# Performance work log

Hardware: AMD Instinct MI355X
Metric: run time of the kernel (lower is better)

## Reference

```python
import jax, jax.numpy as jnp
import numpy as np

B, N, C_IN = 4, 2048, 64
HID, HEADS, NQ = 128, 4, 16
D = HID // HEADS  # per-head dim = 32
NEG_SLOPE = 0.2
MASK_VAL = -1e9


def setup_inputs() -> dict:
    key = jax.random.key(0)
    ks = jax.random.split(key, 8)
    x = jax.random.normal(ks[0], (B, N, C_IN), dtype=jnp.float32)
    adj = jax.random.randint(ks[1], (N, N), 0, 2, dtype=jnp.int32)
    # lin_in: Linear(in_channels, hidden_dim)
    W_in = jax.random.normal(ks[2], (C_IN, HID), dtype=jnp.float32) / np.sqrt(C_IN)
    b_in = jnp.zeros((HID,), dtype=jnp.float32)
    # attention vectors [1, heads, d]
    att_src = jax.random.normal(ks[3], (1, HEADS, D), dtype=jnp.float32) * 0.1
    att_dst = jax.random.normal(ks[4], (1, HEADS, D), dtype=jnp.float32) * 0.1
    # output_head: Linear(num_nodes*hidden_dim, num_qubits)
    W_out = jax.random.normal(ks[5], (N * HID, NQ), dtype=jnp.float32) / np.sqrt(N * HID)
    b_out = jnp.zeros((NQ,), dtype=jnp.float32)
    return {"x": x, "adj": adj, "W_in": W_in, "b_in": b_in,
            "att_src": att_src, "att_dst": att_dst,
            "W_out": W_out, "b_out": b_out}


def reference(x, adj, W_in, b_in, att_src, att_dst, W_out, b_out):
    b, n, _ = x.shape
    h = (x @ W_in + b_in).reshape(b, n, HEADS, D)          # [B,N,H,D]
    alpha_src = jnp.sum(h * att_src, axis=-1)               # [B,N,H]
    alpha_dst = jnp.sum(h * att_dst, axis=-1)               # [B,N,H]
    # additive scores: score[b,i,j,h] = src[b,i,h] + dst[b,j,h]
    scores = alpha_src[:, :, None, :] + alpha_dst[:, None, :, :]  # [B,N,N,H]
    scores = jnp.where(scores >= 0, scores, NEG_SLOPE * scores)   # leaky relu
    mask = (adj == 0)[None, :, :, None]                     # [1,N,N,1]
    scores = jnp.where(mask, MASK_VAL, scores)
    alpha = jax.nn.softmax(scores, axis=2)                  # softmax over neighbors j
    # dropout p=0.0 (eval) -> identity
    out = jnp.einsum('bijh,bjhd->bihd', alpha, h)           # [B,N,H,D]
    out = out.reshape(b, n * HEADS * D)                     # [B, N*HID]
    return out @ W_out + b_out                              # [B, NQ]
```

## Files before the change

kernel.cpp:

```cpp
#include <hip/hip_runtime.h>
#include <math.h>

#define BB 4
#define NN 2048
#define CIN 64
#define HID 128
#define HEADS 4
#define DD 32
#define NQ 16
#define KTOT (NN*HID)
#define CCH 256
#define LOG2E 1.44269504088896340736f
#define NEGBIG -100.0f

typedef __attribute__((ext_vector_type(8))) _Float16 half8;
typedef __attribute__((ext_vector_type(2))) _Float16 half2;
typedef __attribute__((ext_vector_type(4))) float f32x4;

__global__ __launch_bounds__(256) void k_hidden(
    const float* __restrict__ x, const float* __restrict__ W_in,
    const float* __restrict__ b_in, const float* __restrict__ att_src,
    const float* __restrict__ att_dst, _Float16* __restrict__ hH,
    float* __restrict__ srcA, float* __restrict__ dstA)
{
    __shared__ float Wl[CIN * HID];
    __shared__ float xl[16][CIN];
    const int t = threadIdx.x;
    const int jj0 = blockIdx.x * 16;

    {
        const float4* Ws = (const float4*)W_in;
        float4* Wd = (float4*)Wl;
#pragma unroll
        for (int u = 0; u < 8; ++u) Wd[t + 256 * u] = Ws[t + 256 * u];
        ((float4*)&xl[0][0])[t] = ((const float4*)(x + (size_t)jj0 * CIN))[t];
    }
    __syncthreads();

    const int c = t & 127, rg = t >> 7;
    const int b = jj0 >> 11, j0 = jj0 & (NN - 1);
    const int h = c >> 5;

    float acc[8];
    const float bc = b_in[c];
#pragma unroll
    for (int rr = 0; rr < 8; ++rr) acc[rr] = bc;

#pragma unroll
    for (int k4 = 0; k4 < CIN; k4 += 4) {
        const float w0 = Wl[(k4 + 0) * HID + c];
        const float w1 = Wl[(k4 + 1) * HID + c];
        const float w2 = Wl[(k4 + 2) * HID + c];
        const float w3 = Wl[(k4 + 3) * HID + c];
#pragma unroll
        for (int rr = 0; rr < 8; ++rr) {
            const float4 xv = *(const float4*)&xl[rg * 8 + rr][k4];
            acc[rr] = fmaf(xv.w, w3, fmaf(xv.z, w2, fmaf(xv.y, w1, fmaf(xv.x, w0, acc[rr]))));
        }
    }

    half8 hv;
#pragma unroll
    for (int rr = 0; rr < 8; ++rr) hv[rr] = (_Float16)acc[rr];
    *(half8*)(hH + (size_t)(b * HID + c) * NN + j0 + rg * 8) = hv;

    const float as = att_src[c], ad = att_dst[c];
#pragma unroll
    for (int rr = 0; rr < 8; ++rr) {
        float vs = acc[rr] * as, vd = acc[rr] * ad;
#pragma unroll
        for (int m = 16; m >= 1; m >>= 1) {
            vs += __shfl_xor(vs, m, 64);
            vd += __shfl_xor(vd, m, 64);
        }
        if ((t & 31) == 0) {
            srcA[(size_t)(b * HEADS + h) * NN + j0 + rg * 8 + rr] = vs;
            dstA[(size_t)(b * HEADS + h) * NN + j0 + rg * 8 + rr] = vd;
        }
    }
}

__global__ __launch_bounds__(256) void k_adjb(const int* __restrict__ adj,
                                              unsigned* __restrict__ adjb)
{
    const int wid = blockIdx.x * 4 + (threadIdx.x >> 6);
    const int lane = threadIdx.x & 63;
    const int i = wid >> 5;
    const int jc = wid & 31;
    const int a = adj[(size_t)i * NN + jc * 64 + lane];
    const unsigned long long m = __ballot(a != 0);
    if (lane == 0) {
        *(uint2*)(adjb + (size_t)i * (NN / 32) + jc * 2) =
            make_uint2((unsigned)m, (unsigned)(m >> 32));
    }
}

__global__ __launch_bounds__(512, 4) void k_attn(
    const unsigned* __restrict__ adjb, const _Float16* __restrict__ hH,
    const float* __restrict__ srcA, const float* __restrict__ dstA,
    float* __restrict__ attO)
{
    __shared__ float ldst[HEADS][NN];
    __shared__ float redA[8][16][36];
    __shared__ float redS[8][16];

    const int t = threadIdx.x;
    const int lane = t & 63;
    const int w = t >> 6;
    const int h = w & 3;
    const int jh = w >> 2;
    const int b = blockIdx.x >> 7;
    const int i0 = (blockIdx.x & 127) * 16;

    {
        const float4* s4 = (const float4*)(dstA + (size_t)(b * HEADS + h) * NN + jh * 1024);
        float4* d4 = (float4*)&ldst[h][jh * 1024];
#pragma unroll
        for (int u = 0; u < 4; ++u) {
            float4 v = s4[lane + 64 * u];
            v.x *= LOG2E; v.y *= LOG2E; v.z *= LOG2E; v.w *= LOG2E;
            d4[lane + 64 * u] = v;
        }
    }

    const int r16 = lane & 15;
    const int g = lane >> 4;
    const float srci = srcA[(size_t)(b * HEADS + h) * NN + i0 + r16] * LOG2E;
    const uint2* adjrow2 = (const uint2*)(adjb + (size_t)(i0 + r16) * (NN / 32)) + jh * 16;
    const _Float16* bbase = hH + ((size_t)(b * HID) + h * DD + r16) * NN + jh * 1024 + 8 * g;

    f32x4 acc0 = {0.f, 0.f, 0.f, 0.f};
    f32x4 acc1 = {0.f, 0.f, 0.f, 0.f};
    f32x4 accS = {0.f, 0.f, 0.f, 0.f};
    const half8 ones = {(_Float16)1.f, (_Float16)1.f, (_Float16)1.f, (_Float16)1.f,
                        (_Float16)1.f, (_Float16)1.f, (_Float16)1.f, (_Float16)1.f};

    for (int jt2 = 0; jt2 < 1024; jt2 += 64) {
        const uint2 aw2 = adjrow2[jt2 >> 6];
#pragma unroll
        for (int s2 = 0; s2 < 2; ++s2) {
            const int jt = jt2 + 32 * s2;
            const unsigned bits = (s2 ? aw2.y : aw2.x) >> (8 * g);
            const float* dp = &ldst[h][jh * 1024 + jt + 8 * g];
            const float4 dl0 = *(const float4*)dp;
            const float4 dl1 = *(const float4*)(dp + 4);
            const half8 b0 = *(const half8*)(bbase + jt);
            const half8 b1 = *(const half8*)(bbase + 16 * NN + jt);
            const float dv[8] = {dl0.x, dl0.y, dl0.z, dl0.w, dl1.x, dl1.y, dl1.z, dl1.w};
            float wv[8];
#pragma unroll
            for (int e = 0; e < 8; ++e) {
                float s = srci + dv[e];
                s = fmaxf(s, 0.2f * s);
                s = (bits & (1u << e)) ? s : NEGBIG;
                wv[e] = __builtin_amdgcn_exp2f(s);
            }
            const half2 p0 = __builtin_bit_cast(half2, __builtin_amdgcn_cvt_pkrtz(wv[0], wv[1]));
            const half2 p1 = __builtin_bit_cast(half2, __builtin_amdgcn_cvt_pkrtz(wv[2], wv[3]));
            const half2 p2 = __builtin_bit_cast(half2, __builtin_amdgcn_cvt_pkrtz(wv[4], wv[5]));
            const half2 p3 = __builtin_bit_cast(half2, __builtin_amdgcn_cvt_pkrtz(wv[6], wv[7]));
            half8 af;
            af[0] = p0[0]; af[1] = p0[1]; af[2] = p1[0]; af[3] = p1[1];
            af[4] = p2[0]; af[5] = p2[1]; af[6] = p3[0]; af[7] = p3[1];
            acc0 = __builtin_amdgcn_mfma_f32_16x16x32_f16(af, b0, acc0, 0, 0, 0);
            acc1 = __builtin_amdgcn_mfma_f32_16x16x32_f16(af, b1, acc1, 0, 0, 0);
            accS = __builtin_amdgcn_mfma_f32_16x16x32_f16(af, ones, accS, 0, 0, 0);
        }
    }

#pragma unroll
    for (int r = 0; r < 4; ++r) {
        redA[w][4 * g + r][r16]      = acc0[r];
        redA[w][4 * g + r][16 + r16] = acc1[r];
    }
    if (r16 == 0) {
#pragma unroll
        for (int r = 0; r < 4; ++r) redS[w][4 * g + r] = accS[r];
    }
    __syncthreads();

    {
        const int i = t >> 5;
        const int q = t & 31;
        const int h2 = q >> 3;
        const int d0 = (q & 7) * 4;
        const float4 v0 = *(const float4*)&redA[h2][i][d0];
        const float4 v1 = *(const float4*)&redA[h2 + 4][i][d0];
        const float rs = redS[h2][i] + redS[h2 + 4][i];
        const float inv = __builtin_amdgcn_rcpf(rs);
        float4 o;
        o.x = (v0.x + v1.x) * inv; o.y = (v0.y + v1.y) * inv;
        o.z = (v0.z + v1.z) * inv; o.w = (v0.w + v1.w) * inv;
        *(float4*)(attO + (size_t)(b * NN + i0 + i) * HID + h2 * DD + d0) = o;
    }
}

__global__ void k_init(const float* __restrict__ b_out, float* __restrict__ dout)
{
    const int t = threadIdx.x;
    dout[t] = b_out[t & 15];
}

__global__ __launch_bounds__(256) void k_proj(
    const float* __restrict__ attO, const float* __restrict__ W_out,
    float* __restrict__ dout)
{
    const int t = threadIdx.x;
    const int k0 = blockIdx.x * (KTOT / CCH);

    float acc[64];
#pragma unroll
    for (int r = 0; r < 64; ++r) acc[r] = 0.f;

    for (int s = 0; s < (KTOT / CCH) / 256; ++s) {
        const int k = k0 + s * 256 + t;
        float a[4];
#pragma unroll
        for (int b = 0; b < 4; ++b) a[b] = attO[(size_t)b * KTOT + k];
        const float4* wr = (const float4*)(W_out + (size_t)k * NQ);
        float wf[16];
#pragma unroll
        for (int q4 = 0; q4 < 4; ++q4) {
            const float4 w4 = wr[q4];
            wf[q4 * 4 + 0] = w4.x; wf[q4 * 4 + 1] = w4.y;
            wf[q4 * 4 + 2] = w4.z; wf[q4 * 4 + 3] = w4.w;
        }
#pragma unroll
        for (int b = 0; b < 4; ++b)
#pragma unroll
            for (int q = 0; q < 16; ++q)
                acc[b * 16 + q] = fmaf(a[b], wf[q], acc[b * 16 + q]);
    }

    const int lane = t & 63, wave = t >> 6;
    __shared__ float red[4][64];
#pragma unroll
    for (int r = 0; r < 64; ++r) {
        float v = acc[r];
        v += __shfl_down(v, 32, 64);
        v += __shfl_down(v, 16, 64);
        v += __shfl_down(v, 8, 64);
        v += __shfl_down(v, 4, 64);
        v += __shfl_down(v, 2, 64);
        v += __shfl_down(v, 1, 64);
        if (lane == 0) red[wave][r] = v;
    }
    __syncthreads();
    if (t < 64) {
        const float v = red[0][t] + red[1][t] + red[2][t] + red[3][t];
        atomicAdd(&dout[t], v);
    }
}

extern "C" void kernel_launch(void* const* d_in, const int* in_sizes, int n_in,
                              void* d_out, int out_size, void* d_ws, size_t ws_size,
                              hipStream_t stream)
{
    const float* x       = (const float*)d_in[0];
    const int*   adj     = (const int*)d_in[1];
    const float* W_in    = (const float*)d_in[2];
    const float* b_in    = (const float*)d_in[3];
    const float* att_src = (const float*)d_in[4];
    const float* att_dst = (const float*)d_in[5];
    const float* W_out   = (const float*)d_in[6];
    const float* b_out   = (const float*)d_in[7];
    float* out = (float*)d_out;

    float* ws = (float*)d_ws;
    float* attO = ws;
    float* srcA = ws + (size_t)BB * HID * NN;
    float* dstA = srcA + (size_t)BB * HEADS * NN;
    _Float16* hH = (_Float16*)(dstA + (size_t)BB * HEADS * NN);
    unsigned* adjbw = (unsigned*)((char*)hH + sizeof(_Float16) * (size_t)BB * HID * NN);

    k_hidden<<<BB * NN / 16, 256, 0, stream>>>(x, W_in, b_in, att_src, att_dst, hH, srcA, dstA);
    k_adjb<<<NN * (NN / 64) / 4, 256, 0, stream>>>(adj, adjbw);
    k_attn<<<BB * (NN / 16), 512, 0, stream>>>(adjbw, hH, srcA, dstA, attO);
    k_init<<<1, 64, 0, stream>>>(b_out, out);
    k_proj<<<CCH, 256, 0, stream>>>(attO, W_out, out);
}
```

Measured before the change: 88.10 us.

## Split attention over neighbor halves, defer normalization to projection, fold init

The attention kernel's neighbor range is split across two blocks, doubling the grid, and its shared-memory dst staging is removed in favour of direct global loads with prefetched B and dst operands. Each half writes unnormalized fp16 partial outputs plus row sums. The projection kernel then combines both halves, normalizes and applies W_out, using one block per 512 K-elements. The LOG2E scaling moves into k_hidden, and output bias init is folded into k_adjb, removing a launch. The aim is more parallelism and occupancy in attention and fewer launches, at the cost of extra fp16 partial traffic, reduced precision, and many more atomics in the projection.

```diff
diff --git a/kernel.cpp b/kernel.cpp
--- a/kernel.cpp
+++ b/kernel.cpp
@@ -9,11 +9,11 @@
 #define DD 32
 #define NQ 16
 #define KTOT (NN*HID)
-#define CCH 256
 #define LOG2E 1.44269504088896340736f
 #define NEGBIG -100.0f
 
 typedef __attribute__((ext_vector_type(8))) _Float16 half8;
+typedef __attribute__((ext_vector_type(4))) _Float16 half4;
 typedef __attribute__((ext_vector_type(2))) _Float16 half2;
 typedef __attribute__((ext_vector_type(4))) float f32x4;
 
@@ -74,15 +74,18 @@
             vd += __shfl_xor(vd, m, 64);
         }
         if ((t & 31) == 0) {
-            srcA[(size_t)(b * HEADS + h) * NN + j0 + rg * 8 + rr] = vs;
-            dstA[(size_t)(b * HEADS + h) * NN + j0 + rg * 8 + rr] = vd;
+            srcA[(size_t)(b * HEADS + h) * NN + j0 + rg * 8 + rr] = vs * LOG2E;
+            dstA[(size_t)(b * HEADS + h) * NN + j0 + rg * 8 + rr] = vd * LOG2E;
         }
     }
 }
 
 __global__ __launch_bounds__(256) void k_adjb(const int* __restrict__ adj,
-                                              unsigned* __restrict__ adjb)
-{
+                                              unsigned* __restrict__ adjb,
+                                              const float* __restrict__ b_out,
+                                              float* __restrict__ dout)
+{
+    if (blockIdx.x == 0 && threadIdx.x < 64) dout[threadIdx.x] = b_out[threadIdx.x & 15];
     const int wid = blockIdx.x * 4 + (threadIdx.x >> 6);
     const int lane = threadIdx.x & 63;
     const int i = wid >> 5;
@@ -95,12 +98,11 @@
     }
 }
 
-__global__ __launch_bounds__(512, 4) void k_attn(
+__global__ __launch_bounds__(512, 8) void k_attn(
     const unsigned* __restrict__ adjb, const _Float16* __restrict__ hH,
     const float* __restrict__ srcA, const float* __restrict__ dstA,
-    float* __restrict__ attO)
-{
-    __shared__ float ldst[HEADS][NN];
+    _Float16* __restrict__ P, float* __restrict__ S)
+{
     __shared__ float redA[8][16][36];
     __shared__ float redS[8][16];
 
@@ -108,26 +110,18 @@
     const int lane = t & 63;
     const int w = t >> 6;
     const int h = w & 3;
-    const int jh = w >> 2;
-    const int b = blockIdx.x >> 7;
-    const int i0 = (blockIdx.x & 127) * 16;
-
-    {
-        const float4* s4 = (const float4*)(dstA + (size_t)(b * HEADS + h) * NN + jh * 1024);
-        float4* d4 = (float4*)&ldst[h][jh * 1024];
-#pragma unroll
-        for (int u = 0; u < 4; ++u) {
-            float4 v = s4[lane + 64 * u];
-            v.x *= LOG2E; v.y *= LOG2E; v.z *= LOG2E; v.w *= LOG2E;
-            d4[lane + 64 * u] = v;
-        }
-    }
+    const int bx = blockIdx.x;
+    const int jh = bx >> 9;
+    const int b = (bx >> 7) & 3;
+    const int i0 = (bx & 127) * 16;
+    const int jstart = jh * 1024 + (w >> 2) * 512;
 
     const int r16 = lane & 15;
     const int g = lane >> 4;
-    const float srci = srcA[(size_t)(b * HEADS + h) * NN + i0 + r16] * LOG2E;
-    const uint2* adjrow2 = (const uint2*)(adjb + (size_t)(i0 + r16) * (NN / 32)) + jh * 16;
-    const _Float16* bbase = hH + ((size_t)(b * HID) + h * DD + r16) * NN + jh * 1024 + 8 * g;
+    const float srci = srcA[(size_t)(b * HEADS + h) * NN + i0 + r16];
+    const uint2* adjrow2 = (const uint2*)(adjb + (size_t)(i0 + r16) * (NN / 32)) + (jstart >> 6);
+    const _Float16* bbase = hH + ((size_t)(b * HID) + h * DD + r16) * NN + jstart + 8 * g;
+    const float4* dst4 = (const float4*)(dstA + (size_t)(b * HEADS + h) * NN + jstart) + 2 * g;
 
     f32x4 acc0 = {0.f, 0.f, 0.f, 0.f};
     f32x4 acc1 = {0.f, 0.f, 0.f, 0.f};
@@ -135,18 +129,23 @@
     const half8 ones = {(_Float16)1.f, (_Float16)1.f, (_Float16)1.f, (_Float16)1.f,
                         (_Float16)1.f, (_Float16)1.f, (_Float16)1.f, (_Float16)1.f};
 
-    for (int jt2 = 0; jt2 < 1024; jt2 += 64) {
-        const uint2 aw2 = adjrow2[jt2 >> 6];
+    for (int it = 0; it < 8; ++it) {
+        const uint2 aw2 = adjrow2[it];
+        const half8 b0a = *(const half8*)(bbase + it * 64);
+        const half8 b0b = *(const half8*)(bbase + it * 64 + 32);
+        const half8 b1a = *(const half8*)(bbase + 16 * NN + it * 64);
+        const half8 b1b = *(const half8*)(bbase + 16 * NN + it * 64 + 32);
+        const float4 d0a = dst4[it * 16];
+        const float4 d0b = dst4[it * 16 + 1];
+        const float4 d1a = dst4[it * 16 + 8];
+        const float4 d1b = dst4[it * 16 + 9];
+
 #pragma unroll
         for (int s2 = 0; s2 < 2; ++s2) {
-            const int jt = jt2 + 32 * s2;
             const unsigned bits = (s2 ? aw2.y : aw2.x) >> (8 * g);
-            const float* dp = &ldst[h][jh * 1024 + jt + 8 * g];
-            const float4 dl0 = *(const float4*)dp;
-            const float4 dl1 = *(const float4*)(dp + 4);
-            const half8 b0 = *(const half8*)(bbase + jt);
-            const half8 b1 = *(const half8*)(bbase + 16 * NN + jt);
-            const float dv[8] = {dl0.x, dl0.y, dl0.z, dl0.w, dl1.x, dl1.y, dl1.z, dl1.w};
+            const float4 da = s2 ? d1a : d0a;
+            const float4 db = s2 ? d1b : d0b;
+            const float dv[8] = {da.x, da.y, da.z, da.w, db.x, db.y, db.z, db.w};
             float wv[8];
 #pragma unroll
             for (int e = 0; e < 8; ++e) {
@@ -162,8 +161,10 @@
             half8 af;
             af[0] = p0[0]; af[1] = p0[1]; af[2] = p1[0]; af[3] = p1[1];
             af[4] = p2[0]; af[5] = p2[1]; af[6] = p3[0]; af[7] = p3[1];
-            acc0 = __builtin_amdgcn_mfma_f32_16x16x32_f16(af, b0, acc0, 0, 0, 0);
-            acc1 = __builtin_amdgcn_mfma_f32_16x16x32_f16(af, b1, acc1, 0, 0, 0);
+            const half8 bb0 = s2 ? b0b : b0a;
+            const half8 bb1 = s2 ? b1b : b1a;
+            acc0 = __builtin_amdgcn_mfma_f32_16x16x32_f16(af, bb0, acc0, 0, 0, 0);
+            acc1 = __builtin_amdgcn_mfma_f32_16x16x32_f16(af, bb1, acc1, 0, 0, 0);
             accS = __builtin_amdgcn_mfma_f32_16x16x32_f16(af, ones, accS, 0, 0, 0);
         }
     }
@@ -186,50 +187,49 @@
         const int d0 = (q & 7) * 4;
         const float4 v0 = *(const float4*)&redA[h2][i][d0];
         const float4 v1 = *(const float4*)&redA[h2 + 4][i][d0];
-        const float rs = redS[h2][i] + redS[h2 + 4][i];
+        const half2 lo = __builtin_bit_cast(half2, __builtin_amdgcn_cvt_pkrtz(v0.x + v1.x, v0.y + v1.y));
+        const half2 hi = __builtin_bit_cast(half2, __builtin_amdgcn_cvt_pkrtz(v0.z + v1.z, v0.w + v1.w));
+        half4 o; o[0] = lo[0]; o[1] = lo[1]; o[2] = hi[0]; o[3] = hi[1];
+        *(half4*)(P + ((size_t)(jh * BB + b) * NN + i0 + i) * HID + h2 * DD + d0) = o;
+        if ((q & 7) == 0)
+            S[((size_t)(jh * BB + b) * NN + i0 + i) * HEADS + h2] = redS[h2][i] + redS[h2 + 4][i];
+    }
+}
+
+__global__ __launch_bounds__(256) void k_proj(
+    const _Float16* __restrict__ P, const float* __restrict__ S,
+    const float* __restrict__ W_out, float* __restrict__ dout)
+{
+    const int t = threadIdx.x;
+    const int k = blockIdx.x * 512 + t * 2;
+    const int i = k >> 7;
+    const int h = (k >> 5) & 3;
+
+    float wf0[16], wf1[16];
+    {
+        const float4* wr = (const float4*)(W_out + (size_t)k * NQ);
+#pragma unroll
+        for (int q4 = 0; q4 < 4; ++q4) {
+            const float4 a = wr[q4];
+            wf0[q4 * 4 + 0] = a.x; wf0[q4 * 4 + 1] = a.y; wf0[q4 * 4 + 2] = a.z; wf0[q4 * 4 + 3] = a.w;
+            const float4 c = wr[4 + q4];
+            wf1[q4 * 4 + 0] = c.x; wf1[q4 * 4 + 1] = c.y; wf1[q4 * 4 + 2] = c.z; wf1[q4 * 4 + 3] = c.w;
+        }
+    }
+
+    float acc[64];
+#pragma unroll
+    for (int b = 0; b < 4; ++b) {
+        const half2 p0 = *(const half2*)(P + (size_t)b * KTOT + k);
+        const half2 p1 = *(const half2*)(P + (size_t)(BB + b) * KTOT + k);
+        const float rs = S[((size_t)b * NN + i) * HEADS + h] +
+                         S[((size_t)(BB + b) * NN + i) * HEADS + h];
         const float inv = __builtin_amdgcn_rcpf(rs);
-        float4 o;
-        o.x = (v0.x + v1.x) * inv; o.y = (v0.y + v1.y) * inv;
-        o.z = (v0.z + v1.z) * inv; o.w = (v0.w + v1.w) * inv;
-        *(float4*)(attO + (size_t)(b * NN + i0 + i) * HID + h2 * DD + d0) = o;
-    }
-}
-
-__global__ void k_init(const float* __restrict__ b_out, float* __restrict__ dout)
-{
-    const int t = threadIdx.x;
-    dout[t] = b_out[t & 15];
-}
-
-__global__ __launch_bounds__(256) void k_proj(
-    const float* __restrict__ attO, const float* __restrict__ W_out,
-    float* __restrict__ dout)
-{
-    const int t = threadIdx.x;
-    const int k0 = blockIdx.x * (KTOT / CCH);
-
-    float acc[64];
-#pragma unroll
-    for (int r = 0; r < 64; ++r) acc[r] = 0.f;
-
-    for (int s = 0; s < (KTOT / CCH) / 256; ++s) {
-        const int k = k0 + s * 256 + t;
-        float a[4];
-#pragma unroll
-        for (int b = 0; b < 4; ++b) a[b] = attO[(size_t)b * KTOT + k];
-        const float4* wr = (const float4*)(W_out + (size_t)k * NQ);
-        float wf[16];
-#pragma unroll
-        for (int q4 = 0; q4 < 4; ++q4) {
-            const float4 w4 = wr[q4];
-            wf[q4 * 4 + 0] = w4.x; wf[q4 * 4 + 1] = w4.y;
-            wf[q4 * 4 + 2] = w4.z; wf[q4 * 4 + 3] = w4.w;
-        }
-#pragma unroll
-        for (int b = 0; b < 4; ++b)
-#pragma unroll
-            for (int q = 0; q < 16; ++q)
-                acc[b * 16 + q] = fmaf(a[b], wf[q], acc[b * 16 + q]);
+        const float a0 = ((float)p0[0] + (float)p1[0]) * inv;
+        const float a1 = ((float)p0[1] + (float)p1[1]) * inv;
+#pragma unroll
+        for (int q = 0; q < 16; ++q)
+            acc[b * 16 + q] = fmaf(a1, wf1[q], a0 * wf0[q]);
     }
 
     const int lane = t & 63, wave = t >> 6;
@@ -266,16 +266,16 @@
     const float* b_out   = (const float*)d_in[7];
     float* out = (float*)d_out;
 
-    float* ws = (float*)d_ws;
-    float* attO = ws;
-    float* srcA = ws + (size_t)BB * HID * NN;
-    float* dstA = srcA + (size_t)BB * HEADS * NN;
+    char* ws = (char*)d_ws;
+    _Float16* P  = (_Float16*)ws;
+    float* S     = (float*)(ws + sizeof(_Float16) * 2 * (size_t)BB * KTOT);
+    float* srcA  = S + 2 * (size_t)BB * NN * HEADS;
+    float* dstA  = srcA + (size_t)BB * HEADS * NN;
     _Float16* hH = (_Float16*)(dstA + (size_t)BB * HEADS * NN);
-    unsigned* adjbw = (unsigned*)((char*)hH + sizeof(_Float16) * (size_t)BB * HID * NN);
+    unsigned* adjbw = (unsigned*)((char*)hH + sizeof(_Float16) * (size_t)BB * KTOT);
 
     k_hidden<<<BB * NN / 16, 256, 0, stream>>>(x, W_in, b_in, att_src, att_dst, hH, srcA, dstA);
-    k_adjb<<<NN * (NN / 64) / 4, 256, 0, stream>>>(adj, adjbw);
-    k_attn<<<BB * (NN / 16), 512, 0, stream>>>(adjbw, hH, srcA, dstA, attO);
-    k_init<<<1, 64, 0, stream>>>(b_out, out);
-    k_proj<<<CCH, 256, 0, stream>>>(attO, W_out, out);
-}
+    k_adjb<<<NN * (NN / 64) / 4, 256, 0, stream>>>(adj, adjbw, b_out, out);
+    k_attn<<<2 * BB * (NN / 16), 512, 0, stream>>>(adjbw, hH, srcA, dstA, P, S);
+    k_proj<<<KTOT / 512, 256, 0, stream>>>(P, S, W_out, out);
+}
```

After: 98.57 us. 11.9% more time.
